# Kernel optimization log

Measured on AMD Instinct MI355X. Metric: run time of the kernel, lower is better.

## Reference

```python
import jax, jax.numpy as jnp
import numpy as np

DIM = 128
NUM_HEADS = 4
WH, WW = 7, 7
N_TOK = WH * WW  # 49
HEAD_DIM = DIM // NUM_HEADS
SCALE = HEAD_DIM ** (-0.5)
BIAS_TABLE_LEN = (2 * WH - 1) * (2 * WW - 1)  # 169


def _make_relative_position_index():
    coords_h = np.arange(WH)
    coords_w = np.arange(WW)
    coords = np.stack(np.meshgrid(coords_h, coords_w, indexing='ij'))  # (2, Wh, Ww)
    coords_flat = coords.reshape(2, -1)                                # (2, N)
    rel = coords_flat[:, :, None] - coords_flat[:, None, :]            # (2, N, N)
    rel = rel.transpose(1, 2, 0).copy()                                # (N, N, 2)
    rel[:, :, 0] += WH - 1
    rel[:, :, 1] += WW - 1
    rel[:, :, 1] *= 2 * WW - 1
    return rel.sum(-1)  # wait: original multiplies second coord then sums -- matches Swin


def setup_inputs() -> dict:
    key = jax.random.key(0)
    ks = jax.random.split(key, 7)
    B = 4096   # 64 images * 64 windows
    nW = 64    # windows per image
    x = jax.random.normal(ks[0], (B, N_TOK, DIM), dtype=jnp.float32)
    mask = jax.random.normal(ks[1], (nW, N_TOK, N_TOK), dtype=jnp.float32)
    qkv_w = jax.random.normal(ks[2], (3 * DIM, DIM), dtype=jnp.float32) * (DIM ** -0.5)
    qkv_b = jnp.zeros((3 * DIM,), dtype=jnp.float32)
    proj_w = jax.random.normal(ks[3], (DIM, DIM), dtype=jnp.float32) * (DIM ** -0.5)
    proj_b = jnp.zeros((DIM,), dtype=jnp.float32)
    bias_table = jax.random.normal(ks[4], (BIAS_TABLE_LEN, NUM_HEADS), dtype=jnp.float32) * 0.02
    rel_index = jnp.asarray(_make_relative_position_index(), dtype=jnp.int32)  # (N, N)
    return {"x": x, "mask": mask, "qkv_w": qkv_w, "qkv_b": qkv_b,
            "proj_w": proj_w, "proj_b": proj_b, "bias_table": bias_table,
            "rel_index": rel_index}


def reference(x, mask, qkv_w, qkv_b, proj_w, proj_b, bias_table, rel_index):
    B, N, C = x.shape
    nH, hd = NUM_HEADS, HEAD_DIM
    # qkv projection (torch Linear: x @ W^T + b)
    qkv = x @ qkv_w.T + qkv_b                       # (B, N, 3C)
    qkv = qkv.reshape(B, N, 3, nH, hd).transpose(2, 0, 3, 1, 4)  # (3, B, nH, N, hd)
    q, k, v = qkv[0], qkv[1], qkv[2]
    attn = jnp.einsum('bhnd,bhmd->bhnm', q, k) * SCALE  # (B, nH, N, N)
    # relative position bias gather: (N*N,) indices into (L, nH) table -> (nH, N, N)
    bias = bias_table[rel_index.reshape(-1)].reshape(N, N, nH).transpose(2, 0, 1)
    attn = attn + bias[None]
    # per-window mask: B = (B // nW) * nW
    nW = mask.shape[0]
    attn = attn.reshape(B // nW, nW, nH, N, N) + mask[None, :, None]
    attn = attn.reshape(B, nH, N, N)
    attn = jax.nn.softmax(attn, axis=-1)
    out = jnp.einsum('bhnm,bhmd->bhnd', attn, v)    # (B, nH, N, hd)
    out = out.transpose(0, 2, 1, 3).reshape(B, N, C)
    return out @ proj_w.T + proj_b
```

## Files before the change

kernel.cpp:

```cpp
#include <hip/hip_runtime.h>
#include <hip/hip_bf16.h>
#include <stdint.h>

#define NTOK 49
#define DIM  128
#define NH   4
#define QKVN 384
#define SCALE 0.17677669529663687f

typedef __bf16 bfloat_t;
typedef bfloat_t bf16x8 __attribute__((ext_vector_type(8)));
typedef bfloat_t bf16x4 __attribute__((ext_vector_type(4)));
typedef short    s16x4  __attribute__((ext_vector_type(4)));
typedef float    f32x4  __attribute__((ext_vector_type(4)));

#define MFMA32(a, b, c) __builtin_amdgcn_mfma_f32_16x16x32_bf16(a, b, c, 0, 0, 0)
#define MFMA16(a, b, c) __builtin_amdgcn_mfma_f32_16x16x16bf16_1k(a, b, c, 0, 0, 0)

static __device__ __forceinline__ bf16x4 pk4(f32x4 a) {
    bf16x4 r = { (bfloat_t)a[0], (bfloat_t)a[1], (bfloat_t)a[2], (bfloat_t)a[3] };
    return r;
}
static __device__ __forceinline__ s16x4 asi(bf16x4 v) {
    return __builtin_bit_cast(s16x4, v);
}

__global__ void prep_weights(const float* __restrict__ qkvw,
                             const float* __restrict__ projw,
                             bfloat_t* __restrict__ qkvw_b,
                             bfloat_t* __restrict__ projw_b) {
    int i = blockIdx.x * 256 + threadIdx.x;
    if (i < QKVN * DIM) qkvw_b[i] = (bfloat_t)qkvw[i];
    if (i < DIM * DIM)  projw_b[i] = (bfloat_t)projw[i];
}

__global__ void prep_cmb(const float* __restrict__ mask,
                         const float* __restrict__ bias_table,
                         const int* __restrict__ rel_index,
                         float* __restrict__ cmb) {
    int wh = blockIdx.x;
    int w = wh >> 2, h = wh & 3;
    for (int idx = threadIdx.x; idx < 4096; idx += 256) {
        int row = idx >> 6, col = idx & 63;
        float v;
        if (col >= NTOK)      v = -1e30f;
        else if (row >= NTOK) v = 0.f;
        else v = bias_table[rel_index[row * NTOK + col] * NH + h]
               + mask[(w * NTOK + row) * NTOK + col];
        cmb[(size_t)wh * 4096 + idx] = v;
    }
}

__global__ __launch_bounds__(256, 4)
void win_attn(const float* __restrict__ x,
              const float* __restrict__ qkv_b,
              const float* __restrict__ proj_b,
              const bfloat_t* __restrict__ qkvw,
              const bfloat_t* __restrict__ projw,
              const float* __restrict__ cmb,
              float* __restrict__ out, int nw) {
    __shared__ __align__(16) char smem[16384];
    const int b    = blockIdx.x;
    const int tid  = threadIdx.x;
    const int wave = tid >> 6;
    const int lane = tid & 63;
    const int g = lane >> 4;
    const int c = lane & 15;
    const int h = wave;

    {
        const float* xb = x + (size_t)b * (NTOK * DIM);
        #pragma unroll
        for (int i = 0; i < 8; ++i) {
            const int s = tid + i * 256;
            const int row = s >> 5, col4 = (s & 31) * 4;
            f32x4 v = (row < NTOK) ? *(const f32x4*)(xb + row * DIM + col4)
                                   : (f32x4){0.f, 0.f, 0.f, 0.f};
            *(bf16x4*)(smem + row * 256 + ((col4 * 2) ^ ((row & 7) << 4))) = pk4(v);
        }
    }
    __syncthreads();

    #define LDX(t, ks) (*(const bf16x8*)(smem + ((t)*16 + c) * 256 + \
                        (((ks)*64 + g*16) ^ ((c & 7) << 4))))

    bf16x4 qp[2][4], kp[2][4], vp[4][2];

    {
        f32x4 acc[2][4];
        #pragma unroll
        for (int mtd = 0; mtd < 2; ++mtd) {
            const f32x4 qb4 = *(const f32x4*)(qkv_b + h * 32 + mtd * 16 + g * 4);
            #pragma unroll
            for (int nt = 0; nt < 4; ++nt) acc[mtd][nt] = qb4;
        }
        #pragma unroll
        for (int ks = 0; ks < 4; ++ks) {
            bf16x8 w0 = *(const bf16x8*)(qkvw + (h * 32 +  0 + c) * DIM + ks * 32 + g * 8);
            bf16x8 w1 = *(const bf16x8*)(qkvw + (h * 32 + 16 + c) * DIM + ks * 32 + g * 8);
            #pragma unroll
            for (int nt = 0; nt < 4; ++nt) {
                bf16x8 a = LDX(nt, ks);
                acc[0][nt] = MFMA32(w0, a, acc[0][nt]);
                acc[1][nt] = MFMA32(w1, a, acc[1][nt]);
            }
        }
        #pragma unroll
        for (int ds = 0; ds < 2; ++ds)
            #pragma unroll
            for (int nt = 0; nt < 4; ++nt) {
                f32x4 a = acc[ds][nt];
                f32x4 sc = { a[0]*SCALE, a[1]*SCALE, a[2]*SCALE, a[3]*SCALE };
                qp[ds][nt] = pk4(sc);
            }
    }

    {
        f32x4 acc[2][4];
        #pragma unroll
        for (int mtd = 0; mtd < 2; ++mtd) {
            const f32x4 kb4 = *(const f32x4*)(qkv_b + DIM + h * 32 + mtd * 16 + g * 4);
            #pragma unroll
            for (int nt = 0; nt < 4; ++nt) acc[mtd][nt] = kb4;
        }
        #pragma unroll
        for (int ks = 0; ks < 4; ++ks) {
            bf16x8 w0 = *(const bf16x8*)(qkvw + (DIM + h * 32 +  0 + c) * DIM + ks * 32 + g * 8);
            bf16x8 w1 = *(const bf16x8*)(qkvw + (DIM + h * 32 + 16 + c) * DIM + ks * 32 + g * 8);
            #pragma unroll
            for (int nt = 0; nt < 4; ++nt) {
                bf16x8 a = LDX(nt, ks);
                acc[0][nt] = MFMA32(w0, a, acc[0][nt]);
                acc[1][nt] = MFMA32(w1, a, acc[1][nt]);
            }
        }
        #pragma unroll
        for (int ds = 0; ds < 2; ++ds)
            #pragma unroll
            for (int nt = 0; nt < 4; ++nt) kp[ds][nt] = pk4(acc[ds][nt]);
    }

    {
        f32x4 acc[4][2];
        #pragma unroll
        for (int nt = 0; nt < 2; ++nt) {
            const float vb = qkv_b[2 * DIM + h * 32 + nt * 16 + c];
            #pragma unroll
            for (int mt = 0; mt < 4; ++mt) acc[mt][nt] = (f32x4){vb, vb, vb, vb};
        }
        #pragma unroll
        for (int ks = 0; ks < 4; ++ks) {
            bf16x8 w0 = *(const bf16x8*)(qkvw + (2 * DIM + h * 32 +  0 + c) * DIM + ks * 32 + g * 8);
            bf16x8 w1 = *(const bf16x8*)(qkvw + (2 * DIM + h * 32 + 16 + c) * DIM + ks * 32 + g * 8);
            #pragma unroll
            for (int mt = 0; mt < 4; ++mt) {
                bf16x8 a = LDX(mt, ks);
                acc[mt][0] = MFMA32(a, w0, acc[mt][0]);
                acc[mt][1] = MFMA32(a, w1, acc[mt][1]);
            }
        }
        #pragma unroll
        for (int mt = 0; mt < 4; ++mt)
            #pragma unroll
            for (int nt = 0; nt < 2; ++nt) vp[mt][nt] = pk4(acc[mt][nt]);
    }

    bf16x4 pp[4][4];
    float dinv[4];
    {
        const float* cw = cmb + (size_t)((b % nw) * NH + h) * 4096;
        #pragma unroll
        for (int ntq = 0; ntq < 4; ++ntq) {
            f32x4 s[4];
            #pragma unroll
            for (int mtk = 0; mtk < 4; ++mtk)
                s[mtk] = *(const f32x4*)(cw + (ntq * 16 + c) * 64 + mtk * 16 + g * 4);
            #pragma unroll
            for (int mtk = 0; mtk < 4; ++mtk) {
                s[mtk] = MFMA16(asi(kp[0][mtk]), asi(qp[0][ntq]), s[mtk]);
                s[mtk] = MFMA16(asi(kp[1][mtk]), asi(qp[1][ntq]), s[mtk]);
            }
            float m = s[0][0];
            #pragma unroll
            for (int mtk = 0; mtk < 4; ++mtk)
                #pragma unroll
                for (int r = 0; r < 4; ++r) m = fmaxf(m, s[mtk][r]);
            m = fmaxf(m, __shfl_xor(m, 16));
            m = fmaxf(m, __shfl_xor(m, 32));
            float sum = 0.f;
            #pragma unroll
            for (int mtk = 0; mtk < 4; ++mtk)
                #pragma unroll
                for (int r = 0; r < 4; ++r) {
                    float p = __expf(s[mtk][r] - m);
                    s[mtk][r] = p;
                    sum += p;
                }
            sum += __shfl_xor(sum, 16);
            sum += __shfl_xor(sum, 32);
            dinv[ntq] = 1.f / sum;
            #pragma unroll
            for (int mtk = 0; mtk < 4; ++mtk) pp[mtk][ntq] = pk4(s[mtk]);
        }
    }

    f32x4 o[2][4];
    {
        #pragma unroll
        for (int mtd = 0; mtd < 2; ++mtd)
            #pragma unroll
            for (int ntq = 0; ntq < 4; ++ntq) o[mtd][ntq] = (f32x4){0.f, 0.f, 0.f, 0.f};
        #pragma unroll
        for (int mtk = 0; mtk < 4; ++mtk)
            #pragma unroll
            for (int mtd = 0; mtd < 2; ++mtd)
                #pragma unroll
                for (int ntq = 0; ntq < 4; ++ntq)
                    o[mtd][ntq] = MFMA16(asi(vp[mtk][mtd]), asi(pp[mtk][ntq]), o[mtd][ntq]);
        #pragma unroll
        for (int mtd = 0; mtd < 2; ++mtd)
            #pragma unroll
            for (int ntq = 0; ntq < 4; ++ntq)
                #pragma unroll
                for (int r = 0; r < 4; ++r) o[mtd][ntq][r] *= dinv[ntq];
    }

    __syncthreads();
    #pragma unroll
    for (int mtd = 0; mtd < 2; ++mtd)
        #pragma unroll
        for (int ntq = 0; ntq < 4; ++ntq) {
            const int byte = (ntq*16 + c)*256 + ((((h*4 + 2*mtd + (g>>1)) ^ c) & 15) << 4) + ((g&1) << 3);
            *(bf16x4*)(smem + byte) = pk4(o[mtd][ntq]);
        }
    __syncthreads();

    {
        f32x4 po[2][4];
        #pragma unroll
        for (int mtO = 0; mtO < 2; ++mtO) {
            const f32x4 pb4 = *(const f32x4*)(proj_b + wave * 32 + mtO * 16 + g * 4);
            #pragma unroll
            for (int nt = 0; nt < 4; ++nt) po[mtO][nt] = pb4;
        }
        #pragma unroll
        for (int ks = 0; ks < 4; ++ks) {
            bf16x8 w0 = *(const bf16x8*)(projw + (wave * 32 +  0 + c) * DIM + ks * 32 + g * 8);
            bf16x8 w1 = *(const bf16x8*)(projw + (wave * 32 + 16 + c) * DIM + ks * 32 + g * 8);
            bf16x8 aof[4];
            #pragma unroll
            for (int nt = 0; nt < 4; ++nt)
                aof[nt] = *(const bf16x8*)(smem + (nt*16 + c)*256 + ((((ks*4 + g) ^ c) & 15) << 4));
            #pragma unroll
            for (int nt = 0; nt < 4; ++nt) {
                po[0][nt] = MFMA32(w0, aof[nt], po[0][nt]);
                po[1][nt] = MFMA32(w1, aof[nt], po[1][nt]);
            }
        }
        float* og = out + (size_t)b * (NTOK * DIM);
        #pragma unroll
        for (int nt = 0; nt < 4; ++nt) {
            const int tok = nt * 16 + c;
            if (tok < NTOK) {
                #pragma unroll
                for (int mtO = 0; mtO < 2; ++mtO)
                    *(f32x4*)(og + tok * DIM + wave * 32 + mtO * 16 + g * 4) = po[mtO][nt];
            }
        }
    }
    #undef LDX
}

extern "C" void kernel_launch(void* const* d_in, const int* in_sizes, int n_in,
                              void* d_out, int out_size, void* d_ws, size_t ws_size,
                              hipStream_t stream) {
    (void)n_in; (void)out_size; (void)ws_size;
    const float* x          = (const float*)d_in[0];
    const float* mask       = (const float*)d_in[1];
    const float* qkv_w      = (const float*)d_in[2];
    const float* qkv_b      = (const float*)d_in[3];
    const float* proj_w     = (const float*)d_in[4];
    const float* proj_b     = (const float*)d_in[5];
    const float* bias_table = (const float*)d_in[6];
    const int*   rel_index  = (const int*)d_in[7];
    float* out = (float*)d_out;

    char* ws = (char*)d_ws;
    bfloat_t* qkvw_b  = (bfloat_t*)ws;
    bfloat_t* projw_b = (bfloat_t*)(ws + 98304);
    float*    cmb     = (float*)(ws + 131072);

    const int B  = in_sizes[0] / (NTOK * DIM);
    const int nw = in_sizes[1] / (NTOK * NTOK);

    prep_weights<<<dim3((QKVN * DIM + 255) / 256), dim3(256), 0, stream>>>(qkv_w, proj_w, qkvw_b, projw_b);
    prep_cmb<<<dim3(nw * NH), dim3(256), 0, stream>>>(mask, bias_table, rel_index, cmb);
    win_attn<<<dim3(B), dim3(256), 0, stream>>>(x, qkv_b, proj_b, qkvw_b, projw_b, cmb, out, nw);
}
```

Before: 161.3 us.

## Process four windows per block with double-buffered prefetch of next window input

Each block now handles four consecutive windows in a loop instead of one. While the QKV projection of the current window runs, the next window's x tile is loaded into registers, then converted to bf16 and written into a second shared-memory buffer. This is meant to hide global-load latency and amortize block launch overhead. In exchange it doubles shared memory, adds the prefetch registers, and cuts the grid to a quarter as many blocks, which may hurt occupancy and latency hiding across blocks.

```diff
diff --git a/kernel.cpp b/kernel.cpp
--- a/kernel.cpp
+++ b/kernel.cpp
@@ -7,6 +7,7 @@
 #define NH   4
 #define QKVN 384
 #define SCALE 0.17677669529663687f
+#define WPB 4
 
 typedef __bf16 bfloat_t;
 typedef bfloat_t bf16x8 __attribute__((ext_vector_type(8)));
@@ -58,18 +59,22 @@
               const bfloat_t* __restrict__ qkvw,
               const bfloat_t* __restrict__ projw,
               const float* __restrict__ cmb,
-              float* __restrict__ out, int nw) {
-    __shared__ __align__(16) char smem[16384];
-    const int b    = blockIdx.x;
+              float* __restrict__ out, int nw, int Btot) {
+    __shared__ __align__(16) char smem[32768];
     const int tid  = threadIdx.x;
     const int wave = tid >> 6;
     const int lane = tid & 63;
     const int g = lane >> 4;
     const int c = lane & 15;
     const int h = wave;
+    const int wbase = blockIdx.x * WPB;
+
+    const int srow  = tid >> 5;
+    const int scol4 = (tid & 31) * 4;
+    const int sbyte = srow * 256 + ((scol4 * 2) ^ ((srow & 7) << 4));
 
     {
-        const float* xb = x + (size_t)b * (NTOK * DIM);
+        const float* xb = x + (size_t)wbase * (NTOK * DIM);
         #pragma unroll
         for (int i = 0; i < 8; ++i) {
             const int s = tid + i * 256;
@@ -81,194 +86,218 @@
     }
     __syncthreads();
 
-    #define LDX(t, ks) (*(const bf16x8*)(smem + ((t)*16 + c) * 256 + \
-                        (((ks)*64 + g*16) ^ ((c & 7) << 4))))
-
-    bf16x4 qp[2][4], kp[2][4], vp[4][2];
-
-    {
-        f32x4 acc[2][4];
-        #pragma unroll
-        for (int mtd = 0; mtd < 2; ++mtd) {
-            const f32x4 qb4 = *(const f32x4*)(qkv_b + h * 32 + mtd * 16 + g * 4);
-            #pragma unroll
-            for (int nt = 0; nt < 4; ++nt) acc[mtd][nt] = qb4;
-        }
-        #pragma unroll
-        for (int ks = 0; ks < 4; ++ks) {
-            bf16x8 w0 = *(const bf16x8*)(qkvw + (h * 32 +  0 + c) * DIM + ks * 32 + g * 8);
-            bf16x8 w1 = *(const bf16x8*)(qkvw + (h * 32 + 16 + c) * DIM + ks * 32 + g * 8);
+    int cur = 0;
+    for (int w = 0; w < WPB; ++w) {
+        const int b = wbase + w;
+        char* bufc = smem + cur * 16384;
+        char* bufn = smem + (cur ^ 1) * 16384;
+
+        const bool have_next = (w + 1 < WPB) && (b + 1 < Btot);
+        f32x4 pre[8];
+        if (have_next) {
+            const float* xb = x + (size_t)(b + 1) * (NTOK * DIM);
+            #pragma unroll
+            for (int i = 0; i < 8; ++i) {
+                const int s = tid + i * 256;
+                const int row = s >> 5, col4 = (s & 31) * 4;
+                pre[i] = (row < NTOK) ? *(const f32x4*)(xb + row * DIM + col4)
+                                      : (f32x4){0.f, 0.f, 0.f, 0.f};
+            }
+        }
+
+        #define LDX(t, ks) (*(const bf16x8*)(bufc + ((t)*16 + c) * 256 + \
+                            (((ks)*64 + g*16) ^ ((c & 7) << 4))))
+
+        bf16x4 qp[2][4], kp[2][4], vp[4][2];
+
+        {
+            f32x4 acc[2][4];
+            #pragma unroll
+            for (int mtd = 0; mtd < 2; ++mtd) {
+                const f32x4 qb4 = *(const f32x4*)(qkv_b + h * 32 + mtd * 16 + g * 4);
+                #pragma unroll
+                for (int nt = 0; nt < 4; ++nt) acc[mtd][nt] = qb4;
+            }
+            #pragma unroll
+            for (int ks = 0; ks < 4; ++ks) {
+                bf16x8 w0 = *(const bf16x8*)(qkvw + (h * 32 +  0 + c) * DIM + ks * 32 + g * 8);
+                bf16x8 w1 = *(const bf16x8*)(qkvw + (h * 32 + 16 + c) * DIM + ks * 32 + g * 8);
+                #pragma unroll
+                for (int nt = 0; nt < 4; ++nt) {
+                    bf16x8 a = LDX(nt, ks);
+                    acc[0][nt] = MFMA32(w0, a, acc[0][nt]);
+                    acc[1][nt] = MFMA32(w1, a, acc[1][nt]);
+                }
+            }
+            #pragma unroll
+            for (int ds = 0; ds < 2; ++ds)
+                #pragma unroll
+                for (int nt = 0; nt < 4; ++nt) {
+                    f32x4 a = acc[ds][nt];
+                    f32x4 sc = { a[0]*SCALE, a[1]*SCALE, a[2]*SCALE, a[3]*SCALE };
+                    qp[ds][nt] = pk4(sc);
+                }
+        }
+        {
+            f32x4 acc[2][4];
+            #pragma unroll
+            for (int mtd = 0; mtd < 2; ++mtd) {
+                const f32x4 kb4 = *(const f32x4*)(qkv_b + DIM + h * 32 + mtd * 16 + g * 4);
+                #pragma unroll
+                for (int nt = 0; nt < 4; ++nt) acc[mtd][nt] = kb4;
+            }
+            #pragma unroll
+            for (int ks = 0; ks < 4; ++ks) {
+                bf16x8 w0 = *(const bf16x8*)(qkvw + (DIM + h * 32 +  0 + c) * DIM + ks * 32 + g * 8);
+                bf16x8 w1 = *(const bf16x8*)(qkvw + (DIM + h * 32 + 16 + c) * DIM + ks * 32 + g * 8);
+                #pragma unroll
+                for (int nt = 0; nt < 4; ++nt) {
+                    bf16x8 a = LDX(nt, ks);
+                    acc[0][nt] = MFMA32(w0, a, acc[0][nt]);
+                    acc[1][nt] = MFMA32(w1, a, acc[1][nt]);
+                }
+            }
+            #pragma unroll
+            for (int ds = 0; ds < 2; ++ds)
+                #pragma unroll
+                for (int nt = 0; nt < 4; ++nt) kp[ds][nt] = pk4(acc[ds][nt]);
+        }
+        {
+            f32x4 acc[4][2];
+            #pragma unroll
+            for (int nt = 0; nt < 2; ++nt) {
+                const float vb = qkv_b[2 * DIM + h * 32 + nt * 16 + c];
+                #pragma unroll
+                for (int mt = 0; mt < 4; ++mt) acc[mt][nt] = (f32x4){vb, vb, vb, vb};
+            }
+            #pragma unroll
+            for (int ks = 0; ks < 4; ++ks) {
+                bf16x8 w0 = *(const bf16x8*)(qkvw + (2 * DIM + h * 32 +  0 + c) * DIM + ks * 32 + g * 8);
+                bf16x8 w1 = *(const bf16x8*)(qkvw + (2 * DIM + h * 32 + 16 + c) * DIM + ks * 32 + g * 8);
+                #pragma unroll
+                for (int mt = 0; mt < 4; ++mt) {
+                    bf16x8 a = LDX(mt, ks);
+                    acc[mt][0] = MFMA32(a, w0, acc[mt][0]);
+                    acc[mt][1] = MFMA32(a, w1, acc[mt][1]);
+                }
+            }
+            #pragma unroll
+            for (int mt = 0; mt < 4; ++mt)
+                #pragma unroll
+                for (int nt = 0; nt < 2; ++nt) vp[mt][nt] = pk4(acc[mt][nt]);
+        }
+        #undef LDX
+
+        __syncthreads();
+
+        if (have_next) {
+            #pragma unroll
+            for (int i = 0; i < 8; ++i) {
+                const int s = tid + i * 256;
+                const int row = s >> 5, col4 = (s & 31) * 4;
+                *(bf16x4*)(bufn + row * 256 + ((col4 * 2) ^ ((row & 7) << 4))) = pk4(pre[i]);
+            }
+        }
+
+        bf16x4 pp[4][4];
+        float dinv[4];
+        {
+            const float* cw = cmb + (size_t)((b % nw) * NH + h) * 4096;
+            #pragma unroll
+            for (int ntq = 0; ntq < 4; ++ntq) {
+                f32x4 s[4];
+                #pragma unroll
+                for (int mtk = 0; mtk < 4; ++mtk)
+                    s[mtk] = *(const f32x4*)(cw + (ntq * 16 + c) * 64 + mtk * 16 + g * 4);
+                #pragma unroll
+                for (int mtk = 0; mtk < 4; ++mtk) {
+                    s[mtk] = MFMA16(asi(kp[0][mtk]), asi(qp[0][ntq]), s[mtk]);
+                    s[mtk] = MFMA16(asi(kp[1][mtk]), asi(qp[1][ntq]), s[mtk]);
+                }
+                float m = s[0][0];
+                #pragma unroll
+                for (int mtk = 0; mtk < 4; ++mtk)
+                    #pragma unroll
+                    for (int r = 0; r < 4; ++r) m = fmaxf(m, s[mtk][r]);
+                m = fmaxf(m, __shfl_xor(m, 16));
+                m = fmaxf(m, __shfl_xor(m, 32));
+                float sum = 0.f;
+                #pragma unroll
+                for (int mtk = 0; mtk < 4; ++mtk)
+                    #pragma unroll
+                    for (int r = 0; r < 4; ++r) {
+                        float p = __expf(s[mtk][r] - m);
+                        s[mtk][r] = p;
+                        sum += p;
+                    }
+                sum += __shfl_xor(sum, 16);
+                sum += __shfl_xor(sum, 32);
+                dinv[ntq] = 1.f / sum;
+                #pragma unroll
+                for (int mtk = 0; mtk < 4; ++mtk) pp[mtk][ntq] = pk4(s[mtk]);
+            }
+        }
+        {
+            f32x4 o[2][4];
+            #pragma unroll
+            for (int mtd = 0; mtd < 2; ++mtd)
+                #pragma unroll
+                for (int ntq = 0; ntq < 4; ++ntq) o[mtd][ntq] = (f32x4){0.f, 0.f, 0.f, 0.f};
+            #pragma unroll
+            for (int mtk = 0; mtk < 4; ++mtk)
+                #pragma unroll
+                for (int mtd = 0; mtd < 2; ++mtd)
+                    #pragma unroll
+                    for (int ntq = 0; ntq < 4; ++ntq)
+                        o[mtd][ntq] = MFMA16(asi(vp[mtk][mtd]), asi(pp[mtk][ntq]), o[mtd][ntq]);
+            #pragma unroll
+            for (int mtd = 0; mtd < 2; ++mtd)
+                #pragma unroll
+                for (int ntq = 0; ntq < 4; ++ntq) {
+                    f32x4 a = o[mtd][ntq];
+                    f32x4 sc = { a[0]*dinv[ntq], a[1]*dinv[ntq], a[2]*dinv[ntq], a[3]*dinv[ntq] };
+                    const int byte = (ntq*16 + c)*256 + ((((h*4 + 2*mtd + (g>>1)) ^ c) & 15) << 4) + ((g&1) << 3);
+                    *(bf16x4*)(bufc + byte) = pk4(sc);
+                }
+        }
+
+        __syncthreads();
+
+        {
+            f32x4 po[2][4];
+            #pragma unroll
+            for (int mtO = 0; mtO < 2; ++mtO) {
+                const f32x4 pb4 = *(const f32x4*)(proj_b + wave * 32 + mtO * 16 + g * 4);
+                #pragma unroll
+                for (int nt = 0; nt < 4; ++nt) po[mtO][nt] = pb4;
+            }
+            #pragma unroll
+            for (int ks = 0; ks < 4; ++ks) {
+                bf16x8 w0 = *(const bf16x8*)(projw + (wave * 32 +  0 + c) * DIM + ks * 32 + g * 8);
+                bf16x8 w1 = *(const bf16x8*)(projw + (wave * 32 + 16 + c) * DIM + ks * 32 + g * 8);
+                bf16x8 aof[4];
+                #pragma unroll
+                for (int nt = 0; nt < 4; ++nt)
+                    aof[nt] = *(const bf16x8*)(bufc + (nt*16 + c)*256 + ((((ks*4 + g) ^ c) & 15) << 4));
+                #pragma unroll
+                for (int nt = 0; nt < 4; ++nt) {
+                    po[0][nt] = MFMA32(w0, aof[nt], po[0][nt]);
+                    po[1][nt] = MFMA32(w1, aof[nt], po[1][nt]);
+                }
+            }
+            float* og = out + (size_t)b * (NTOK * DIM);
             #pragma unroll
             for (int nt = 0; nt < 4; ++nt) {
-                bf16x8 a = LDX(nt, ks);
-                acc[0][nt] = MFMA32(w0, a, acc[0][nt]);
-                acc[1][nt] = MFMA32(w1, a, acc[1][nt]);
-            }
-        }
-        #pragma unroll
-        for (int ds = 0; ds < 2; ++ds)
-            #pragma unroll
-            for (int nt = 0; nt < 4; ++nt) {
-                f32x4 a = acc[ds][nt];
-                f32x4 sc = { a[0]*SCALE, a[1]*SCALE, a[2]*SCALE, a[3]*SCALE };
-                qp[ds][nt] = pk4(sc);
-            }
+                const int tok = nt * 16 + c;
+                if (tok < NTOK) {
+                    #pragma unroll
+                    for (int mtO = 0; mtO < 2; ++mtO)
+                        *(f32x4*)(og + tok * DIM + wave * 32 + mtO * 16 + g * 4) = po[mtO][nt];
+                }
+            }
+        }
+        cur ^= 1;
     }
-
-    {
-        f32x4 acc[2][4];
-        #pragma unroll
-        for (int mtd = 0; mtd < 2; ++mtd) {
-            const f32x4 kb4 = *(const f32x4*)(qkv_b + DIM + h * 32 + mtd * 16 + g * 4);
-            #pragma unroll
-            for (int nt = 0; nt < 4; ++nt) acc[mtd][nt] = kb4;
-        }
-        #pragma unroll
-        for (int ks = 0; ks < 4; ++ks) {
-            bf16x8 w0 = *(const bf16x8*)(qkvw + (DIM + h * 32 +  0 + c) * DIM + ks * 32 + g * 8);
-            bf16x8 w1 = *(const bf16x8*)(qkvw + (DIM + h * 32 + 16 + c) * DIM + ks * 32 + g * 8);
-            #pragma unroll
-            for (int nt = 0; nt < 4; ++nt) {
-                bf16x8 a = LDX(nt, ks);
-                acc[0][nt] = MFMA32(w0, a, acc[0][nt]);
-                acc[1][nt] = MFMA32(w1, a, acc[1][nt]);
-            }
-        }
-        #pragma unroll
-        for (int ds = 0; ds < 2; ++ds)
-            #pragma unroll
-            for (int nt = 0; nt < 4; ++nt) kp[ds][nt] = pk4(acc[ds][nt]);
-    }
-
-    {
-        f32x4 acc[4][2];
-        #pragma unroll
-        for (int nt = 0; nt < 2; ++nt) {
-            const float vb = qkv_b[2 * DIM + h * 32 + nt * 16 + c];
-            #pragma unroll
-            for (int mt = 0; mt < 4; ++mt) acc[mt][nt] = (f32x4){vb, vb, vb, vb};
-        }
-        #pragma unroll
-        for (int ks = 0; ks < 4; ++ks) {
-            bf16x8 w0 = *(const bf16x8*)(qkvw + (2 * DIM + h * 32 +  0 + c) * DIM + ks * 32 + g * 8);
-            bf16x8 w1 = *(const bf16x8*)(qkvw + (2 * DIM + h * 32 + 16 + c) * DIM + ks * 32 + g * 8);
-            #pragma unroll
-            for (int mt = 0; mt < 4; ++mt) {
-                bf16x8 a = LDX(mt, ks);
-                acc[mt][0] = MFMA32(a, w0, acc[mt][0]);
-                acc[mt][1] = MFMA32(a, w1, acc[mt][1]);
-            }
-        }
-        #pragma unroll
-        for (int mt = 0; mt < 4; ++mt)
-            #pragma unroll
-            for (int nt = 0; nt < 2; ++nt) vp[mt][nt] = pk4(acc[mt][nt]);
-    }
-
-    bf16x4 pp[4][4];
-    float dinv[4];
-    {
-        const float* cw = cmb + (size_t)((b % nw) * NH + h) * 4096;
-        #pragma unroll
-        for (int ntq = 0; ntq < 4; ++ntq) {
-            f32x4 s[4];
-            #pragma unroll
-            for (int mtk = 0; mtk < 4; ++mtk)
-                s[mtk] = *(const f32x4*)(cw + (ntq * 16 + c) * 64 + mtk * 16 + g * 4);
-            #pragma unroll
-            for (int mtk = 0; mtk < 4; ++mtk) {
-                s[mtk] = MFMA16(asi(kp[0][mtk]), asi(qp[0][ntq]), s[mtk]);
-                s[mtk] = MFMA16(asi(kp[1][mtk]), asi(qp[1][ntq]), s[mtk]);
-            }
-            float m = s[0][0];
-            #pragma unroll
-            for (int mtk = 0; mtk < 4; ++mtk)
-                #pragma unroll
-                for (int r = 0; r < 4; ++r) m = fmaxf(m, s[mtk][r]);
-            m = fmaxf(m, __shfl_xor(m, 16));
-            m = fmaxf(m, __shfl_xor(m, 32));
-            float sum = 0.f;
-            #pragma unroll
-            for (int mtk = 0; mtk < 4; ++mtk)
-                #pragma unroll
-                for (int r = 0; r < 4; ++r) {
-                    float p = __expf(s[mtk][r] - m);
-                    s[mtk][r] = p;
-                    sum += p;
-                }
-            sum += __shfl_xor(sum, 16);
-            sum += __shfl_xor(sum, 32);
-            dinv[ntq] = 1.f / sum;
-            #pragma unroll
-            for (int mtk = 0; mtk < 4; ++mtk) pp[mtk][ntq] = pk4(s[mtk]);
-        }
-    }
-
-    f32x4 o[2][4];
-    {
-        #pragma unroll
-        for (int mtd = 0; mtd < 2; ++mtd)
-            #pragma unroll
-            for (int ntq = 0; ntq < 4; ++ntq) o[mtd][ntq] = (f32x4){0.f, 0.f, 0.f, 0.f};
-        #pragma unroll
-        for (int mtk = 0; mtk < 4; ++mtk)
-            #pragma unroll
-            for (int mtd = 0; mtd < 2; ++mtd)
-                #pragma unroll
-                for (int ntq = 0; ntq < 4; ++ntq)
-                    o[mtd][ntq] = MFMA16(asi(vp[mtk][mtd]), asi(pp[mtk][ntq]), o[mtd][ntq]);
-        #pragma unroll
-        for (int mtd = 0; mtd < 2; ++mtd)
-            #pragma unroll
-            for (int ntq = 0; ntq < 4; ++ntq)
-                #pragma unroll
-                for (int r = 0; r < 4; ++r) o[mtd][ntq][r] *= dinv[ntq];
-    }
-
-    __syncthreads();
-    #pragma unroll
-    for (int mtd = 0; mtd < 2; ++mtd)
-        #pragma unroll
-        for (int ntq = 0; ntq < 4; ++ntq) {
-            const int byte = (ntq*16 + c)*256 + ((((h*4 + 2*mtd + (g>>1)) ^ c) & 15) << 4) + ((g&1) << 3);
-            *(bf16x4*)(smem + byte) = pk4(o[mtd][ntq]);
-        }
-    __syncthreads();
-
-    {
-        f32x4 po[2][4];
-        #pragma unroll
-        for (int mtO = 0; mtO < 2; ++mtO) {
-            const f32x4 pb4 = *(const f32x4*)(proj_b + wave * 32 + mtO * 16 + g * 4);
-            #pragma unroll
-            for (int nt = 0; nt < 4; ++nt) po[mtO][nt] = pb4;
-        }
-        #pragma unroll
-        for (int ks = 0; ks < 4; ++ks) {
-            bf16x8 w0 = *(const bf16x8*)(projw + (wave * 32 +  0 + c) * DIM + ks * 32 + g * 8);
-            bf16x8 w1 = *(const bf16x8*)(projw + (wave * 32 + 16 + c) * DIM + ks * 32 + g * 8);
-            bf16x8 aof[4];
-            #pragma unroll
-            for (int nt = 0; nt < 4; ++nt)
-                aof[nt] = *(const bf16x8*)(smem + (nt*16 + c)*256 + ((((ks*4 + g) ^ c) & 15) << 4));
-            #pragma unroll
-            for (int nt = 0; nt < 4; ++nt) {
-                po[0][nt] = MFMA32(w0, aof[nt], po[0][nt]);
-                po[1][nt] = MFMA32(w1, aof[nt], po[1][nt]);
-            }
-        }
-        float* og = out + (size_t)b * (NTOK * DIM);
-        #pragma unroll
-        for (int nt = 0; nt < 4; ++nt) {
-            const int tok = nt * 16 + c;
-            if (tok < NTOK) {
-                #pragma unroll
-                for (int mtO = 0; mtO < 2; ++mtO)
-                    *(f32x4*)(og + tok * DIM + wave * 32 + mtO * 16 + g * 4) = po[mtO][nt];
-            }
-        }
-    }
-    #undef LDX
 }
 
 extern "C" void kernel_launch(void* const* d_in, const int* in_sizes, int n_in,
@@ -295,5 +324,5 @@
 
     prep_weights<<<dim3((QKVN * DIM + 255) / 256), dim3(256), 0, stream>>>(qkv_w, proj_w, qkvw_b, projw_b);
     prep_cmb<<<dim3(nw * NH), dim3(256), 0, stream>>>(mask, bias_table, rel_index, cmb);
-    win_attn<<<dim3(B), dim3(256), 0, stream>>>(x, qkv_b, proj_b, qkvw_b, projw_b, cmb, out, nw);
-}
+    win_attn<<<dim3((B + WPB - 1) / WPB), dim3(256), 0, stream>>>(x, qkv_b, proj_b, qkvw_b, projw_b, cmb, out, nw, B);
+}
```

Result: slower. 437.8 us (+171.4%).
